# Kernel tuning notes

Hardware: AMD Instinct MI355X
Metric: run time of the kernel (lower is better)

The kernel has to match this reference:

```python
import jax, jax.numpy as jnp
import numpy as np

N_NODES = 40000
N_EDGES = 640000
D = 128
L = 3
EPS_NORM = 1e-12  # F.normalize eps


def setup_inputs() -> dict:
    key = jax.random.key(0)
    ks = jax.random.split(key, 12)
    s = 1.0 / np.sqrt(D)  # keep activations in a sane range
    x = jax.random.normal(ks[0], (N_NODES, D), dtype=jnp.float32)
    edge_index = jax.random.randint(ks[1], (2, N_EDGES), 0, N_NODES, dtype=jnp.int64)
    return {
        "x": x,
        "edge_index": edge_index,
        "Wk": jax.random.normal(ks[2], (L, D, D), dtype=jnp.float32) * s,
        "bk": jax.random.normal(ks[3], (L, D), dtype=jnp.float32) * s,
        "Wq": jax.random.normal(ks[4], (L, D, D), dtype=jnp.float32) * s,
        "bq": jax.random.normal(ks[5], (L, D), dtype=jnp.float32) * s,
        "Wv": jax.random.normal(ks[6], (L, D, D), dtype=jnp.float32) * s,
        "bv": jax.random.normal(ks[7], (L, D), dtype=jnp.float32) * s,
        "Ws": jax.random.normal(ks[8], (L, D, D), dtype=jnp.float32) * s,
        "gamma": jnp.ones((L, D), dtype=jnp.float32),
        "beta": jnp.zeros((L, D), dtype=jnp.float32),
    }


def _l2norm(h, axis):
    n = jnp.sqrt(jnp.sum(h * h, axis=axis, keepdims=True))
    return h / jnp.maximum(n, EPS_NORM)


def reference(x, edge_index, Wk, bk, Wq, bq, Wv, bv, Ws, gamma, beta):
    src = edge_index[0]  # message source j
    dst = edge_index[1]  # message target i
    n = x.shape[0]
    h = x
    for l in range(Wk.shape[0]):  # fixed small num_layers
        x_in = h
        # ResGatedGraphConv: out_i = W_skip x_i + sum_j sigmoid(k_i + q_j) * v_j
        k = x_in @ Wk[l].T + bk[l]
        q = x_in @ Wq[l].T + bq[l]
        v = x_in @ Wv[l].T + bv[l]
        msg = jax.nn.sigmoid(k[dst] + q[src]) * v[src]          # [E, D]
        agg = jax.ops.segment_sum(msg, dst, num_segments=n)     # [N, D]
        out = agg + x_in @ Ws[l].T                              # no conv bias (has_batch_norm)
        # BatchNorm1d in eval mode with running_mean=0, running_var=1
        out = out * gamma[l] + beta[l]
        out = jax.nn.relu(out)
        out = _l2norm(out, axis=1)        # per-layer has_l2_norm
        h = x_in + out                    # skipsum
    return _l2norm(h, axis=-1)            # final_l2_norm
```

## Files before the change

### kernel.cpp

```cpp
#include <hip/hip_runtime.h>
#include <math.h>

#define NN 40000
#define NE 640000
#define DD 128
#define NL 3
#define SCAN_NBLK ((NN + 255) / 256)
#define NEG_LOG2E -1.4426950408889634f

typedef short s16x8 __attribute__((ext_vector_type(8)));
typedef float f32x4 __attribute__((ext_vector_type(4)));
typedef unsigned short ushort_t;

__device__ __forceinline__ ushort_t f2bf(float f) {
    unsigned int u = __float_as_uint(f);
    u = (u + 0x7FFFu + ((u >> 16) & 1u)) >> 16;
    return (ushort_t)u;
}
__device__ __forceinline__ float bf2f(ushort_t h) {
    return __uint_as_float(((unsigned int)h) << 16);
}

__global__ void convert_hist_kernel(const int* __restrict__ ei,
                                    int* __restrict__ srcs, int* __restrict__ dsts,
                                    int* __restrict__ count) {
    __shared__ int sh_is64;
    if (threadIdx.x == 0) {
        int is64 = 1;
        for (int k = 0; k < 32; ++k)
            if (ei[2 * k + 1] != 0) { is64 = 0; break; }
        sh_is64 = is64;
    }
    __syncthreads();
    int e = blockIdx.x * blockDim.x + threadIdx.x;
    if (e >= NE) return;
    int s, d;
    if (sh_is64) {
        s = ei[2 * e];
        d = ei[2 * (NE + e)];
    } else {
        s = ei[e];
        d = ei[NE + e];
    }
    srcs[e] = s;
    dsts[e] = d;
    atomicAdd(&count[d], 1);
}

__global__ __launch_bounds__(256) void scan1_kernel(const int* __restrict__ count,
                                                    int* __restrict__ row_ptr,
                                                    int* __restrict__ blocksum) {
    __shared__ int tmp[256];
    int t = threadIdx.x;
    int i = blockIdx.x * 256 + t;
    int v = (i < NN) ? count[i] : 0;
    tmp[t] = v;
    __syncthreads();
    for (int off = 1; off < 256; off <<= 1) {
        int u = (t >= off) ? tmp[t - off] : 0;
        __syncthreads();
        tmp[t] += u;
        __syncthreads();
    }
    if (i < NN) row_ptr[i] = tmp[t] - v;
    if (t == 255) blocksum[blockIdx.x] = tmp[255];
}

__global__ __launch_bounds__(256) void scan2_kernel(const int* __restrict__ blocksum,
                                                    int* __restrict__ blockoff) {
    __shared__ int tmp[256];
    int t = threadIdx.x;
    int v = (t < SCAN_NBLK) ? blocksum[t] : 0;
    tmp[t] = v;
    __syncthreads();
    for (int off = 1; off < 256; off <<= 1) {
        int u = (t >= off) ? tmp[t - off] : 0;
        __syncthreads();
        tmp[t] += u;
        __syncthreads();
    }
    if (t < SCAN_NBLK) blockoff[t] = tmp[t] - v;
}

__global__ void scan3_kernel(int* __restrict__ row_ptr, const int* __restrict__ blockoff,
                             int* __restrict__ cursor) {
    int i = blockIdx.x * blockDim.x + threadIdx.x;
    if (i >= NN) return;
    int r = row_ptr[i] + blockoff[i >> 8];
    row_ptr[i] = r;
    cursor[i] = r;
    if (i == 0) row_ptr[NN] = NE;
}

__global__ void scatter_kernel(const int* __restrict__ srcs, const int* __restrict__ dsts,
                               int* __restrict__ cursor, int* __restrict__ csr_src) {
    int e = blockIdx.x * blockDim.x + threadIdx.x;
    if (e >= NE) return;
    int i = dsts[e];
    int pos = atomicAdd(&cursor[i], 1);
    csr_src[pos] = srcs[e];
}

__global__ void cvt_x_kernel(const float* __restrict__ x, ushort_t* __restrict__ xb) {
    int i = blockIdx.x * blockDim.x + threadIdx.x;
    if (i >= NN * DD / 8) return;
    const float* p = x + (size_t)i * 8;
    s16x8 o;
#pragma unroll
    for (int j = 0; j < 8; ++j) o[j] = (short)f2bf(p[j]);
    *(s16x8*)&xb[(size_t)i * 8] = o;
}

__global__ void cvt_w_kernel(const float* __restrict__ Wk, const float* __restrict__ Wq,
                             const float* __restrict__ Wv, const float* __restrict__ Ws,
                             ushort_t* __restrict__ wall) {
    int g = blockIdx.x * blockDim.x + threadIdx.x;
    if (g >= NL * 4 * DD * DD / 8) return;
    size_t flat = (size_t)g * 8;
    int l = (int)(flat / (4 * DD * DD));
    int r = (int)(flat % (4 * DD * DD));
    int m = r / (DD * DD);
    int o = r % (DD * DD);
    const float* src;
    switch (m) {
        case 0: src = Wk; break;
        case 1: src = Wq; break;
        case 2: src = Wv; break;
        default: src = Ws; break;
    }
    const float* p = src + (size_t)l * DD * DD + o;
    s16x8 ov;
#pragma unroll
    for (int j = 0; j < 8; ++j) ov[j] = (short)f2bf(p[j]);
    *(s16x8*)&wall[flat] = ov;
}

__global__ __launch_bounds__(256) void gemm4_mfma(
    const ushort_t* __restrict__ xb,
    const ushort_t* __restrict__ wall,
    const float* __restrict__ bk, const float* __restrict__ bq,
    const float* __restrict__ bv,
    ushort_t* __restrict__ y,
    int layer) {
    __shared__ ushort_t wlds[DD * DD];

    const int t = threadIdx.x;
    const int w = t >> 6;
    const int lane = t & 63;
    const int row0 = blockIdx.x * 64;

    const int arow = row0 + w * 16 + (lane & 15);
    const ushort_t* ap = xb + (size_t)arow * DD + ((lane >> 4) << 3);
    s16x8 afrag[4];
#pragma unroll
    for (int kb = 0; kb < 4; ++kb) afrag[kb] = *(const s16x8*)(ap + kb * 32);

    const int dlow = lane & 15;
    const int dbase = dlow * 256;
    const int swz = (lane & 7) << 4;
    const int g16 = (lane >> 4) << 4;

    unsigned int qs[8][2];

    for (int m = 0; m < 4; ++m) {
        if (m) __syncthreads();
        const ushort_t* wsrc = wall + (((size_t)layer * 4 + m) << 14);
#pragma unroll
        for (int p = 0; p < 8; ++p) {
            int g = p * 256 + t;
            int d = g >> 4;
            int s = g & 15;
            int byteoff = d * 256 + ((s * 16) ^ ((d & 7) << 4));
            *(s16x8*)((char*)wlds + byteoff) = *(const s16x8*)(wsrc + (size_t)g * 8);
        }
        __syncthreads();

        f32x4 acc[8];
#pragma unroll
        for (int ct = 0; ct < 8; ++ct) acc[ct] = (f32x4){0.f, 0.f, 0.f, 0.f};

#pragma unroll
        for (int kb = 0; kb < 4; ++kb) {
#pragma unroll
            for (int ct = 0; ct < 8; ++ct) {
                s16x8 bfrag = *(const s16x8*)((char*)wlds + ct * 4096 + dbase +
                                              ((kb * 64 + g16) ^ swz));
                acc[ct] = __builtin_amdgcn_mfma_f32_16x16x32_bf16(afrag[kb], bfrag,
                                                                  acc[ct], 0, 0, 0);
            }
        }

        const int rbase = row0 + w * 16 + ((lane >> 4) << 2);
#pragma unroll
        for (int ct = 0; ct < 8; ++ct) {
            int c0 = ct * 16 + dlow;
            if (m == 0) {
                float bval = bk[layer * DD + c0];
#pragma unroll
                for (int j = 0; j < 4; ++j)
                    y[(size_t)(rbase + j) * 512 + c0] = f2bf((acc[ct][j] + bval) * NEG_LOG2E);
            } else if (m == 1) {
                float bval = bq[layer * DD + c0];
                qs[ct][0] = (unsigned int)f2bf((acc[ct][0] + bval) * NEG_LOG2E) |
                            ((unsigned int)f2bf((acc[ct][1] + bval) * NEG_LOG2E) << 16);
                qs[ct][1] = (unsigned int)f2bf((acc[ct][2] + bval) * NEG_LOG2E) |
                            ((unsigned int)f2bf((acc[ct][3] + bval) * NEG_LOG2E) << 16);
            } else if (m == 2) {
                float bval = bv[layer * DD + c0];
#pragma unroll
                for (int j = 0; j < 4; ++j) {
                    unsigned int q16 = (qs[ct][j >> 1] >> ((j & 1) * 16)) & 0xFFFFu;
                    unsigned int val = q16 | ((unsigned int)f2bf(acc[ct][j] + bval) << 16);
                    *(unsigned int*)&y[(size_t)(rbase + j) * 512 + 128 + 2 * c0] = val;
                }
            } else {
#pragma unroll
                for (int j = 0; j < 4; ++j)
                    y[(size_t)(rbase + j) * 512 + 384 + c0] = f2bf(acc[ct][j]);
            }
        }
    }
}

__global__ __launch_bounds__(256) void agg_kernel(
    const float* __restrict__ hin,
    const ushort_t* __restrict__ kqvs,
    const int* __restrict__ row_ptr,
    const int* __restrict__ csr_src,
    const float* __restrict__ gamma, const float* __restrict__ beta,
    float* __restrict__ hout, ushort_t* __restrict__ xb_next,
    int layer, int final_norm) {
    int wid = __builtin_amdgcn_readfirstlane(
        (int)((blockIdx.x * blockDim.x + threadIdx.x) >> 6));
    if (wid >= NN) return;
    int lane = threadIdx.x & 63;
    int d0 = lane * 2;

    const ushort_t* base_i = kqvs + ((unsigned)wid << 9);
    ushort2 kraw = *(const ushort2*)&base_i[d0];
    ushort2 sraw = *(const ushort2*)&base_i[384 + d0];
    float kx = bf2f(kraw.x), ky = bf2f(kraw.y);
    float ax = bf2f(sraw.x), ay = bf2f(sraw.y);

    const unsigned qvoff = 128u + 4u * (unsigned)lane;
    int s = row_ptr[wid];
    int e = row_ptr[wid + 1];
    int idx = s;

#define GATE(wrd, KK, AA)                                                    \
    do {                                                                     \
        float qf = __uint_as_float((wrd) << 16);                             \
        float vf = __uint_as_float((wrd) & 0xFFFF0000u);                     \
        float g = __builtin_amdgcn_rcpf(1.0f +                               \
                    __builtin_amdgcn_exp2f(KK + qf));                        \
        AA += g * vf;                                                        \
    } while (0)

    while (idx + 8 <= e) {
        uint2 wv[8];
#pragma unroll
        for (int u = 0; u < 8; ++u) {
            unsigned off = ((unsigned)csr_src[idx + u] << 9) + qvoff;
            wv[u] = *(const uint2*)&kqvs[off];
        }
#pragma unroll
        for (int u = 0; u < 8; ++u) {
            GATE(wv[u].x, kx, ax);
            GATE(wv[u].y, ky, ay);
        }
        idx += 8;
    }
    while (idx + 2 <= e) {
        uint2 w0, w1;
        {
            unsigned off0 = ((unsigned)csr_src[idx] << 9) + qvoff;
            unsigned off1 = ((unsigned)csr_src[idx + 1] << 9) + qvoff;
            w0 = *(const uint2*)&kqvs[off0];
            w1 = *(const uint2*)&kqvs[off1];
        }
        GATE(w0.x, kx, ax);
        GATE(w0.y, ky, ay);
        GATE(w1.x, kx, ax);
        GATE(w1.y, ky, ay);
        idx += 2;
    }
    if (idx < e) {
        unsigned off = ((unsigned)csr_src[idx] << 9) + qvoff;
        uint2 w0 = *(const uint2*)&kqvs[off];
        GATE(w0.x, kx, ax);
        GATE(w0.y, ky, ay);
    }
#undef GATE

    float gx = gamma[layer * DD + d0], gy = gamma[layer * DD + d0 + 1];
    float btx = beta[layer * DD + d0], bty = beta[layer * DD + d0 + 1];
    float rx = fmaxf(ax * gx + btx, 0.f);
    float ry = fmaxf(ay * gy + bty, 0.f);

    float ss = rx * rx + ry * ry;
#pragma unroll
    for (int m = 1; m < 64; m <<= 1) ss += __shfl_xor(ss, m);
    float inv = __builtin_amdgcn_rcpf(fmaxf(sqrtf(ss), 1e-12f));

    float2 xin = *(const float2*)&hin[(size_t)wid * DD + d0];
    float hx = xin.x + rx * inv;
    float hy = xin.y + ry * inv;

    if (final_norm) {
        float s2 = hx * hx + hy * hy;
#pragma unroll
        for (int m = 1; m < 64; m <<= 1) s2 += __shfl_xor(s2, m);
        float inv2 = __builtin_amdgcn_rcpf(fmaxf(sqrtf(s2), 1e-12f));
        hx *= inv2;
        hy *= inv2;
    }
    float2 o;
    o.x = hx;
    o.y = hy;
    *(float2*)&hout[(size_t)wid * DD + d0] = o;
    if (xb_next) {
        ushort2 ob;
        ob.x = f2bf(hx);
        ob.y = f2bf(hy);
        *(ushort2*)&xb_next[(size_t)wid * DD + d0] = ob;
    }
}

extern "C" void kernel_launch(void* const* d_in, const int* in_sizes, int n_in,
                              void* d_out, int out_size, void* d_ws, size_t ws_size,
                              hipStream_t stream) {
    const float* x     = (const float*)d_in[0];
    const int*   ei    = (const int*)d_in[1];
    const float* Wk    = (const float*)d_in[2];
    const float* bk    = (const float*)d_in[3];
    const float* Wq    = (const float*)d_in[4];
    const float* bq    = (const float*)d_in[5];
    const float* Wv    = (const float*)d_in[6];
    const float* bv    = (const float*)d_in[7];
    const float* Ws    = (const float*)d_in[8];
    const float* gamma = (const float*)d_in[9];
    const float* beta  = (const float*)d_in[10];
    float* out = (float*)d_out;

    float* hb0 = (float*)d_ws;
    float* hb1 = hb0 + (size_t)NN * DD;
    ushort_t* kqvs = (ushort_t*)(hb1 + (size_t)NN * DD);
    ushort_t* xb   = kqvs + (size_t)NN * 4 * DD;
    ushort_t* wall = xb + (size_t)NN * DD;
    int* srcs     = (int*)(wall + (size_t)NL * 4 * DD * DD);
    int* dsts     = srcs + NE;
    int* count    = dsts + NE;
    int* cursor   = count + NN;
    int* row_ptr  = cursor + NN;
    int* csr_src  = row_ptr + (NN + 1);
    int* blocksum = csr_src + NE;
    int* blockoff = blocksum + SCAN_NBLK;

    hipMemsetAsync(count, 0, NN * sizeof(int), stream);
    convert_hist_kernel<<<(NE + 255) / 256, 256, 0, stream>>>(ei, srcs, dsts, count);
    scan1_kernel<<<SCAN_NBLK, 256, 0, stream>>>(count, row_ptr, blocksum);
    scan2_kernel<<<1, 256, 0, stream>>>(blocksum, blockoff);
    scan3_kernel<<<(NN + 255) / 256, 256, 0, stream>>>(row_ptr, blockoff, cursor);
    scatter_kernel<<<(NE + 255) / 256, 256, 0, stream>>>(srcs, dsts, cursor, csr_src);

    cvt_x_kernel<<<(NN * DD / 8 + 255) / 256, 256, 0, stream>>>(x, xb);
    cvt_w_kernel<<<(NL * 4 * DD * DD / 8 + 255) / 256, 256, 0, stream>>>(Wk, Wq, Wv, Ws, wall);

    for (int l = 0; l < NL; ++l) {
        const float* hin = (l == 0) ? x : (l == 1 ? hb0 : hb1);
        float* hout = (l == 2) ? out : (l == 0 ? hb0 : hb1);
        ushort_t* xb_next = (l == 2) ? nullptr : xb;
        gemm4_mfma<<<NN / 64, 256, 0, stream>>>(xb, wall, bk, bq, bv, kqvs, l);
        agg_kernel<<<(NN * 64) / 256, 256, 0, stream>>>(hin, kqvs, row_ptr, csr_src, gamma,
                                                        beta, hout, xb_next, l,
                                                        (l == NL - 1) ? 1 : 0);
    }
}
```

Before: 278.1 us.

## Split k/skip and q/v buffers, pre-shift CSR indices, drop fp32 residual stream

The fused per-node [k|qv|s] row is split into a compact k/skip buffer and a dense interleaved q/v gather buffer with a 512-byte stride. CSR source indices are pre-shifted so the gather needs no shift. The fp32 hidden-state ping-pong buffers are removed and the residual is read from the bf16 copy, which saves fp32 traffic but lowers the precision of the skip path. Nontemporal stores and loads are added for data that is streamed once.

```diff
diff --git a/kernel.cpp b/kernel.cpp
--- a/kernel.cpp
+++ b/kernel.cpp
@@ -10,6 +10,7 @@
 
 typedef short s16x8 __attribute__((ext_vector_type(8)));
 typedef float f32x4 __attribute__((ext_vector_type(4)));
+typedef float f32x2 __attribute__((ext_vector_type(2)));
 typedef unsigned short ushort_t;
 
 __device__ __forceinline__ ushort_t f2bf(float f) {
@@ -98,7 +99,7 @@
     if (e >= NE) return;
     int i = dsts[e];
     int pos = atomicAdd(&cursor[i], 1);
-    csr_src[pos] = srcs[e];
+    csr_src[pos] = srcs[e] << 9;
 }
 
 __global__ void cvt_x_kernel(const float* __restrict__ x, ushort_t* __restrict__ xb) {
@@ -140,7 +141,7 @@
     const ushort_t* __restrict__ wall,
     const float* __restrict__ bk, const float* __restrict__ bq,
     const float* __restrict__ bv,
-    ushort_t* __restrict__ y,
+    ushort_t* __restrict__ ks, ushort_t* __restrict__ gat,
     int layer) {
     __shared__ ushort_t wlds[DD * DD];
 
@@ -198,7 +199,9 @@
                 float bval = bk[layer * DD + c0];
 #pragma unroll
                 for (int j = 0; j < 4; ++j)
-                    y[(size_t)(rbase + j) * 512 + c0] = f2bf((acc[ct][j] + bval) * NEG_LOG2E);
+                    __builtin_nontemporal_store(
+                        f2bf((acc[ct][j] + bval) * NEG_LOG2E),
+                        &ks[(size_t)(rbase + j) * 256 + c0]);
             } else if (m == 1) {
                 float bval = bq[layer * DD + c0];
                 qs[ct][0] = (unsigned int)f2bf((acc[ct][0] + bval) * NEG_LOG2E) |
@@ -211,24 +214,27 @@
                 for (int j = 0; j < 4; ++j) {
                     unsigned int q16 = (qs[ct][j >> 1] >> ((j & 1) * 16)) & 0xFFFFu;
                     unsigned int val = q16 | ((unsigned int)f2bf(acc[ct][j] + bval) << 16);
-                    *(unsigned int*)&y[(size_t)(rbase + j) * 512 + 128 + 2 * c0] = val;
+                    *(unsigned int*)&gat[(size_t)(rbase + j) * 256 + 2 * c0] = val;
                 }
             } else {
 #pragma unroll
                 for (int j = 0; j < 4; ++j)
-                    y[(size_t)(rbase + j) * 512 + 384 + c0] = f2bf(acc[ct][j]);
+                    __builtin_nontemporal_store(
+                        f2bf(acc[ct][j]),
+                        &ks[(size_t)(rbase + j) * 256 + 128 + c0]);
             }
         }
     }
 }
 
 __global__ __launch_bounds__(256) void agg_kernel(
-    const float* __restrict__ hin,
-    const ushort_t* __restrict__ kqvs,
+    const ushort_t* __restrict__ ks,
+    const ushort_t* __restrict__ gat,
     const int* __restrict__ row_ptr,
     const int* __restrict__ csr_src,
     const float* __restrict__ gamma, const float* __restrict__ beta,
-    float* __restrict__ hout, ushort_t* __restrict__ xb_next,
+    ushort_t* __restrict__ xb,
+    float* __restrict__ out_f32,
     int layer, int final_norm) {
     int wid = __builtin_amdgcn_readfirstlane(
         (int)((blockIdx.x * blockDim.x + threadIdx.x) >> 6));
@@ -236,32 +242,35 @@
     int lane = threadIdx.x & 63;
     int d0 = lane * 2;
 
-    const ushort_t* base_i = kqvs + ((unsigned)wid << 9);
-    ushort2 kraw = *(const ushort2*)&base_i[d0];
-    ushort2 sraw = *(const ushort2*)&base_i[384 + d0];
-    float kx = bf2f(kraw.x), ky = bf2f(kraw.y);
-    float ax = bf2f(sraw.x), ay = bf2f(sraw.y);
-
-    const unsigned qvoff = 128u + 4u * (unsigned)lane;
+    const ushort_t* ksp = ks + ((unsigned)wid << 8);
+    unsigned kword = __builtin_nontemporal_load((const unsigned*)&ksp[d0]);
+    unsigned sword = __builtin_nontemporal_load((const unsigned*)&ksp[128 + d0]);
+    float kx = __uint_as_float(kword << 16);
+    float ky = __uint_as_float(kword & 0xFFFF0000u);
+    float ax = __uint_as_float(sword << 16);
+    float ay = __uint_as_float(sword & 0xFFFF0000u);
+
+    const char* gbase = (const char*)gat;
+    const unsigned qvoff = 8u * (unsigned)lane;
     int s = row_ptr[wid];
     int e = row_ptr[wid + 1];
     int idx = s;
 
-#define GATE(wrd, KK, AA)                                                    \
-    do {                                                                     \
-        float qf = __uint_as_float((wrd) << 16);                             \
-        float vf = __uint_as_float((wrd) & 0xFFFF0000u);                     \
-        float g = __builtin_amdgcn_rcpf(1.0f +                               \
-                    __builtin_amdgcn_exp2f(KK + qf));                        \
-        AA += g * vf;                                                        \
+#define GATE(wrd, KK, AA)                                                     \
+    do {                                                                      \
+        float qf = __uint_as_float((wrd) << 16);                              \
+        float vf = __uint_as_float((wrd) & 0xFFFF0000u);                      \
+        float g = __builtin_amdgcn_rcpf(1.0f +                                \
+                    __builtin_amdgcn_exp2f(KK + qf));                         \
+        AA = fmaf(g, vf, AA);                                                 \
     } while (0)
 
     while (idx + 8 <= e) {
         uint2 wv[8];
 #pragma unroll
         for (int u = 0; u < 8; ++u) {
-            unsigned off = ((unsigned)csr_src[idx + u] << 9) + qvoff;
-            wv[u] = *(const uint2*)&kqvs[off];
+            unsigned b = (unsigned)csr_src[idx + u];
+            wv[u] = *(const uint2*)(gbase + b + qvoff);
         }
 #pragma unroll
         for (int u = 0; u < 8; ++u) {
@@ -271,13 +280,10 @@
         idx += 8;
     }
     while (idx + 2 <= e) {
-        uint2 w0, w1;
-        {
-            unsigned off0 = ((unsigned)csr_src[idx] << 9) + qvoff;
-            unsigned off1 = ((unsigned)csr_src[idx + 1] << 9) + qvoff;
-            w0 = *(const uint2*)&kqvs[off0];
-            w1 = *(const uint2*)&kqvs[off1];
-        }
+        unsigned b0 = (unsigned)csr_src[idx];
+        unsigned b1 = (unsigned)csr_src[idx + 1];
+        uint2 w0 = *(const uint2*)(gbase + b0 + qvoff);
+        uint2 w1 = *(const uint2*)(gbase + b1 + qvoff);
         GATE(w0.x, kx, ax);
         GATE(w0.y, ky, ay);
         GATE(w1.x, kx, ax);
@@ -285,8 +291,8 @@
         idx += 2;
     }
     if (idx < e) {
-        unsigned off = ((unsigned)csr_src[idx] << 9) + qvoff;
-        uint2 w0 = *(const uint2*)&kqvs[off];
+        unsigned b0 = (unsigned)csr_src[idx];
+        uint2 w0 = *(const uint2*)(gbase + b0 + qvoff);
         GATE(w0.x, kx, ax);
         GATE(w0.y, ky, ay);
     }
@@ -302,27 +308,22 @@
     for (int m = 1; m < 64; m <<= 1) ss += __shfl_xor(ss, m);
     float inv = __builtin_amdgcn_rcpf(fmaxf(sqrtf(ss), 1e-12f));
 
-    float2 xin = *(const float2*)&hin[(size_t)wid * DD + d0];
-    float hx = xin.x + rx * inv;
-    float hy = xin.y + ry * inv;
+    unsigned xw = *(const unsigned*)&xb[((unsigned)wid << 7) + d0];
+    float hx = __uint_as_float(xw << 16) + rx * inv;
+    float hy = __uint_as_float(xw & 0xFFFF0000u) + ry * inv;
 
     if (final_norm) {
         float s2 = hx * hx + hy * hy;
 #pragma unroll
         for (int m = 1; m < 64; m <<= 1) s2 += __shfl_xor(s2, m);
         float inv2 = __builtin_amdgcn_rcpf(fmaxf(sqrtf(s2), 1e-12f));
-        hx *= inv2;
-        hy *= inv2;
-    }
-    float2 o;
-    o.x = hx;
-    o.y = hy;
-    *(float2*)&hout[(size_t)wid * DD + d0] = o;
-    if (xb_next) {
-        ushort2 ob;
-        ob.x = f2bf(hx);
-        ob.y = f2bf(hy);
-        *(ushort2*)&xb_next[(size_t)wid * DD + d0] = ob;
+        f32x2 o;
+        o.x = hx * inv2;
+        o.y = hy * inv2;
+        __builtin_nontemporal_store(o, (f32x2*)&out_f32[(size_t)wid * DD + d0]);
+    } else {
+        unsigned ob = (unsigned)f2bf(hx) | ((unsigned)f2bf(hy) << 16);
+        *(unsigned*)&xb[((unsigned)wid << 7) + d0] = ob;
     }
 }
 
@@ -342,10 +343,9 @@
     const float* beta  = (const float*)d_in[10];
     float* out = (float*)d_out;
 
-    float* hb0 = (float*)d_ws;
-    float* hb1 = hb0 + (size_t)NN * DD;
-    ushort_t* kqvs = (ushort_t*)(hb1 + (size_t)NN * DD);
-    ushort_t* xb   = kqvs + (size_t)NN * 4 * DD;
+    ushort_t* ks  = (ushort_t*)d_ws;
+    ushort_t* gat = ks + (size_t)NN * 256;
+    ushort_t* xb  = gat + (size_t)NN * 256;
     ushort_t* wall = xb + (size_t)NN * DD;
     int* srcs     = (int*)(wall + (size_t)NL * 4 * DD * DD);
     int* dsts     = srcs + NE;
@@ -356,7 +356,7 @@
     int* blocksum = csr_src + NE;
     int* blockoff = blocksum + SCAN_NBLK;
 
-    hipMemsetAsync(count, 0, NN * sizeof(int), stream);
+    (void)hipMemsetAsync(count, 0, NN * sizeof(int), stream);
     convert_hist_kernel<<<(NE + 255) / 256, 256, 0, stream>>>(ei, srcs, dsts, count);
     scan1_kernel<<<SCAN_NBLK, 256, 0, stream>>>(count, row_ptr, blocksum);
     scan2_kernel<<<1, 256, 0, stream>>>(blocksum, blockoff);
@@ -367,12 +367,9 @@
     cvt_w_kernel<<<(NL * 4 * DD * DD / 8 + 255) / 256, 256, 0, stream>>>(Wk, Wq, Wv, Ws, wall);
 
     for (int l = 0; l < NL; ++l) {
-        const float* hin = (l == 0) ? x : (l == 1 ? hb0 : hb1);
-        float* hout = (l == 2) ? out : (l == 0 ? hb0 : hb1);
-        ushort_t* xb_next = (l == 2) ? nullptr : xb;
-        gemm4_mfma<<<NN / 64, 256, 0, stream>>>(xb, wall, bk, bq, bv, kqvs, l);
-        agg_kernel<<<(NN * 64) / 256, 256, 0, stream>>>(hin, kqvs, row_ptr, csr_src, gamma,
-                                                        beta, hout, xb_next, l,
-                                                        (l == NL - 1) ? 1 : 0);
-    }
-}
+        gemm4_mfma<<<NN / 64, 256, 0, stream>>>(xb, wall, bk, bq, bv, ks, gat, l);
+        agg_kernel<<<(NN * 64) / 256, 256, 0, stream>>>(
+            ks, gat, row_ptr, csr_src, gamma, beta, xb,
+            (l == NL - 1) ? out : nullptr, l, (l == NL - 1) ? 1 : 0);
+    }
+}
```

Result: no change. 282.0 us (+1.4%).
